# Performance work log

Hardware: AMD Instinct MI355X
Metric: run time of the kernel (lower is better)

Reference implementation:

```python
import jax, jax.numpy as jnp
import numpy as np

DIM = 1024
HEADS = 16
HEAD_DIM = DIM // HEADS
HIDDEN = 4 * DIM
SCALE = HEAD_DIM ** -0.5
EPS = 1e-5


def _layernorm(x, g, b):
    mu = jnp.mean(x, axis=-1, keepdims=True)
    var = jnp.mean(jnp.square(x - mu), axis=-1, keepdims=True)
    return (x - mu) * jax.lax.rsqrt(var + EPS) * g + b


def setup_inputs() -> dict:
    key = jax.random.key(0)
    ks = jax.random.split(key, 8)
    B, N, C = 4, 2048, DIM
    s = 0.02
    return {
        "x": jax.random.normal(ks[0], (B, N, C), dtype=jnp.float32),
        "ln1_g": jnp.ones((C,), jnp.float32),
        "ln1_b": jnp.zeros((C,), jnp.float32),
        "qkv_w": jax.random.normal(ks[1], (3 * C, C), jnp.float32) * s,
        "proj_w": jax.random.normal(ks[2], (C, C), jnp.float32) * s,
        "proj_b": jnp.zeros((C,), jnp.float32),
        "ln2_g": jnp.ones((C,), jnp.float32),
        "ln2_b": jnp.zeros((C,), jnp.float32),
        "fc1_w": jax.random.normal(ks[3], (HIDDEN, C), jnp.float32) * s,
        "fc1_b": jnp.zeros((HIDDEN,), jnp.float32),
        "fc2_w": jax.random.normal(ks[4], (C, HIDDEN), jnp.float32) * s,
        "fc2_b": jnp.zeros((C,), jnp.float32),
    }


def reference(x, ln1_g, ln1_b, qkv_w, proj_w, proj_b, ln2_g, ln2_b, fc1_w, fc1_b, fc2_w, fc2_b):
    B, N, C = x.shape
    # --- attention branch ---
    h = _layernorm(x, ln1_g, ln1_b)
    qkv = h @ qkv_w.T                                  # [B,N,3C]
    qkv = qkv.reshape(B, N, 3, HEADS, HEAD_DIM)
    q = qkv[:, :, 0].transpose(0, 2, 1, 3) * SCALE      # [B,H,N,D]
    k = qkv[:, :, 1].transpose(0, 2, 1, 3)
    v = qkv[:, :, 2].transpose(0, 2, 1, 3)
    attn = jax.nn.softmax(jnp.einsum('bhqd,bhkd->bhqk', q, k), axis=-1)
    o = jnp.einsum('bhqk,bhkd->bhqd', attn, v)          # [B,H,N,D]
    o = o.transpose(0, 2, 1, 3).reshape(B, N, C)
    x = x + (o @ proj_w.T + proj_b)
    # --- MLP branch ---
    h2 = _layernorm(x, ln2_g, ln2_b)
    h2 = jax.nn.gelu(h2 @ fc1_w.T + fc1_b, approximate=False)
    x = x + (h2 @ fc2_w.T + fc2_b)
    return x
```

## Files before the change

kernel.cpp:

```cpp
#include <hip/hip_runtime.h>
#include <math.h>

typedef __bf16 bf16;
typedef __attribute__((ext_vector_type(8))) __bf16 bf16x8;
typedef __attribute__((ext_vector_type(4))) __bf16 bf16x4;
typedef __attribute__((ext_vector_type(4))) float floatx4;

#define MFMA(a, b, c) __builtin_amdgcn_mfma_f32_16x16x32_bf16((a), (b), (c), 0, 0, 0)

__device__ __forceinline__ void async_load16(const bf16* g, bf16* l) {
    __builtin_amdgcn_global_load_lds((const __attribute__((address_space(1))) void*)(g),
                                     (__attribute__((address_space(3))) void*)(l), 16, 0, 0);
}

__global__ __launch_bounds__(256) void cast4_kernel(const float* __restrict__ a0,
                                                    const float* __restrict__ a1,
                                                    const float* __restrict__ a2,
                                                    const float* __restrict__ a3,
                                                    bf16* __restrict__ o0,
                                                    bf16* __restrict__ o1,
                                                    bf16* __restrict__ o2,
                                                    bf16* __restrict__ o3) {
    long i = (long)blockIdx.x * 256 + threadIdx.x;
    const float* in;
    bf16* out;
    long off;
    if (i < 393216) { in = a0; out = o0; off = i; }
    else if (i < 524288) { in = a1; out = o1; off = i - 393216; }
    else if (i < 1048576) { in = a2; out = o2; off = i - 524288; }
    else { in = a3; out = o3; off = i - 1048576; }
    const float4 a = ((const float4*)in)[2 * off];
    const float4 b = ((const float4*)in)[2 * off + 1];
    bf16x8 o;
    o[0] = (bf16)a.x; o[1] = (bf16)a.y; o[2] = (bf16)a.z; o[3] = (bf16)a.w;
    o[4] = (bf16)b.x; o[5] = (bf16)b.y; o[6] = (bf16)b.z; o[7] = (bf16)b.w;
    *(bf16x8*)(out + off * 8) = o;
}

__global__ __launch_bounds__(256) void ln_kernel(const float* __restrict__ x,
                                                 const float* __restrict__ g,
                                                 const float* __restrict__ b,
                                                 bf16* __restrict__ out) {
    const int row = blockIdx.x;
    const int tid = threadIdx.x;
    const float4 v = ((const float4*)(x + (long)row * 1024))[tid];
    float s  = v.x + v.y + v.z + v.w;
    float s2 = v.x * v.x + v.y * v.y + v.z * v.z + v.w * v.w;
#pragma unroll
    for (int off = 32; off > 0; off >>= 1) {
        s  += __shfl_xor(s, off, 64);
        s2 += __shfl_xor(s2, off, 64);
    }
    __shared__ float red[8];
    const int wave = tid >> 6, lane = tid & 63;
    if (lane == 0) { red[wave] = s; red[wave + 4] = s2; }
    __syncthreads();
    const float ts  = red[0] + red[1] + red[2] + red[3];
    const float ts2 = red[4] + red[5] + red[6] + red[7];
    const float mu   = ts * (1.0f / 1024.0f);
    const float rstd = rsqrtf(ts2 * (1.0f / 1024.0f) - mu * mu + 1e-5f);
    const float4 gg = ((const float4*)g)[tid];
    const float4 bb = ((const float4*)b)[tid];
    bf16x4 o;
    o[0] = (bf16)((v.x - mu) * rstd * gg.x + bb.x);
    o[1] = (bf16)((v.y - mu) * rstd * gg.y + bb.y);
    o[2] = (bf16)((v.z - mu) * rstd * gg.z + bb.z);
    o[3] = (bf16)((v.w - mu) * rstd * gg.w + bb.w);
    *(bf16x4*)(out + (long)row * 1024 + tid * 4) = o;
}

template <int EPI>
__global__ __launch_bounds__(256, 3)
void gemm_bt(const bf16* __restrict__ A, const bf16* __restrict__ B,
             const float* __restrict__ bias, const float* __restrict__ resid,
             void* __restrict__ Cout, bf16* __restrict__ vtout, int M, int N, int K) {
    __shared__ __align__(16) bf16 sA[128 * 64];
    __shared__ __align__(16) bf16 sB[128 * 64];
    const int tid  = threadIdx.x;
    const int lane = tid & 63;
    const int wave = tid >> 6;
    const int wm = (wave >> 1) << 6;
    const int wn = (wave & 1) << 6;
    const int c15 = lane & 15;
    const int kq  = lane >> 4;
    const int c7  = lane & 7;
    const long tileM = (long)blockIdx.y * 128;
    const long tileN = (long)blockIdx.x * 128;

    floatx4 acc[4][4] = {};

    const int srow = tid >> 3;
    const int scol = ((tid & 7) ^ (srow & 7)) * 8;
    const bf16* Abase = A + (tileM + srow) * (long)K + scol;
    const bf16* Bbase = B + (tileN + srow) * (long)K + scol;
    bf16* sAw = sA + tid * 8;
    bf16* sBw = sB + tid * 8;

    for (int k0 = 0; k0 < K; k0 += 64) {
        __syncthreads();
#pragma unroll
        for (int it = 0; it < 4; ++it) {
            async_load16(Abase + (long)it * 32 * K + k0, sAw + it * 2048);
            async_load16(Bbase + (long)it * 32 * K + k0, sBw + it * 2048);
        }
        __syncthreads();
#pragma unroll
        for (int kk = 0; kk < 2; ++kk) {
            bf16x8 a[4], b[4];
#pragma unroll
            for (int i = 0; i < 4; ++i) {
                const int ch = ((kk << 2) + kq) ^ c7;
                a[i] = *(const bf16x8*)(sA + (wm + i * 16 + c15) * 64 + ch * 8);
                b[i] = *(const bf16x8*)(sB + (wn + i * 16 + c15) * 64 + ch * 8);
            }
#pragma unroll
            for (int i = 0; i < 4; ++i)
#pragma unroll
                for (int j = 0; j < 4; ++j)
                    acc[i][j] = MFMA(a[i], b[j], acc[i][j]);
        }
    }

#pragma unroll
    for (int i = 0; i < 4; ++i)
#pragma unroll
        for (int j = 0; j < 4; ++j) {
            if (EPI == 3 && tileN >= 2048) {
                const long gnv  = tileN - 2048 + wn + j * 16 + c15;
                const long tokb = tileM + wm + i * 16 + kq * 4;
                const long row  = ((tokb >> 11) << 10) + gnv;
                bf16x4 ov;
#pragma unroll
                for (int r = 0; r < 4; ++r) ov[r] = (bf16)acc[i][j][r];
                *(bf16x4*)(vtout + row * 2048 + (tokb & 2047)) = ov;
            } else {
#pragma unroll
                for (int r = 0; r < 4; ++r) {
                    const long gm = tileM + wm + i * 16 + kq * 4 + r;
                    const long gn = tileN + wn + j * 16 + c15;
                    const float v = acc[i][j][r];
                    if (EPI == 0 || EPI == 3) {
                        ((bf16*)Cout)[gm * N + gn] = (bf16)v;
                    } else if (EPI == 1) {
                        ((float*)Cout)[gm * N + gn] = v + bias[gn] + resid[gm * N + gn];
                    } else {
                        const float t = v + bias[gn];
                        ((bf16*)Cout)[gm * N + gn] =
                            (bf16)(0.5f * t * (1.0f + erff(t * 0.70710678118654752f)));
                    }
                }
            }
        }
}

__global__ __launch_bounds__(256, 4)
void attn_kernel(const bf16* __restrict__ qkv, const bf16* __restrict__ vt,
                 bf16* __restrict__ o) {
    __shared__ __align__(16) bf16 sK[64 * 64];
    __shared__ __align__(16) bf16 sV[64 * 64];
    __shared__ __align__(16) bf16 sP[8][16 * 72];
    const int bh = blockIdx.x, b = bh >> 4, h = bh & 15;
    const int q0 = blockIdx.y * 128;
    const int tid = threadIdx.x, lane = tid & 63, wave = tid >> 6;
    const int c15 = lane & 15, kq = lane >> 4, c7 = lane & 7;

    bf16x8 qf[2][2];
#pragma unroll
    for (int t = 0; t < 2; ++t) {
        const bf16* qrow =
            qkv + ((long)(b * 2048 + q0 + wave * 32 + t * 16 + c15)) * 3072 + h * 64;
#pragma unroll
        for (int kk = 0; kk < 2; ++kk) {
            const bf16x8 raw = *(const bf16x8*)(qrow + kk * 32 + kq * 8);
            bf16x8 sc;
#pragma unroll
            for (int e = 0; e < 8; ++e) sc[e] = (bf16)((float)raw[e] * 0.18033688f);
            qf[t][kk] = sc;
        }
    }

    floatx4 oacc[2][4] = {};
    float l_s[2] = {0.f, 0.f};

    const bf16* kbase = qkv + ((long)b * 2048) * 3072 + 1024 + h * 64;
    const bf16* vbase = vt + (long)bh * 64 * 2048;

    const int srow = tid >> 3;
    const int scol = ((tid & 7) ^ (srow & 7)) * 8;
    bf16* sKw = sK + tid * 8;
    bf16* sVw = sV + tid * 8;
    bf16* sP0 = sP[wave * 2];
    bf16* sP1 = sP[wave * 2 + 1];

    for (int kv0 = 0; kv0 < 2048; kv0 += 64) {
        __syncthreads();
#pragma unroll
        for (int it = 0; it < 2; ++it) {
            async_load16(kbase + (long)(kv0 + it * 32 + srow) * 3072 + scol, sKw + it * 2048);
            async_load16(vbase + (long)(it * 32 + srow) * 2048 + kv0 + scol, sVw + it * 2048);
        }
        __syncthreads();

        floatx4 s0[4], s1[4];
#pragma unroll
        for (int j = 0; j < 4; ++j) {
            const bf16x8 k0 = *(const bf16x8*)(sK + (j * 16 + c15) * 64 + ((kq ^ c7) * 8));
            const bf16x8 k1 = *(const bf16x8*)(sK + (j * 16 + c15) * 64 + (((4 | kq) ^ c7) * 8));
            floatx4 a0 = {0.f, 0.f, 0.f, 0.f}, a1 = {0.f, 0.f, 0.f, 0.f};
            a0 = MFMA(k0, qf[0][0], a0);
            a0 = MFMA(k1, qf[0][1], a0);
            a1 = MFMA(k0, qf[1][0], a1);
            a1 = MFMA(k1, qf[1][1], a1);
            s0[j] = a0;
            s1[j] = a1;
        }

#pragma unroll
        for (int t = 0; t < 2; ++t) {
            floatx4* s = (t == 0) ? s0 : s1;
            bf16* sPt = (t == 0) ? sP0 : sP1;
            float rs = 0.f;
#pragma unroll
            for (int j = 0; j < 4; ++j) {
                const float p0 = __builtin_amdgcn_exp2f(s[j][0]);
                const float p1 = __builtin_amdgcn_exp2f(s[j][1]);
                const float p2 = __builtin_amdgcn_exp2f(s[j][2]);
                const float p3 = __builtin_amdgcn_exp2f(s[j][3]);
                rs += (p0 + p1) + (p2 + p3);
                bf16x4 pk;
                pk[0] = (bf16)p0; pk[1] = (bf16)p1; pk[2] = (bf16)p2; pk[3] = (bf16)p3;
                *(bf16x4*)(sPt + c15 * 72 + j * 16 + kq * 4) = pk;
            }
            l_s[t] += rs;
        }

        bf16x8 pf[2][2];
#pragma unroll
        for (int t = 0; t < 2; ++t) {
            bf16* sPt = (t == 0) ? sP0 : sP1;
            pf[t][0] = *(const bf16x8*)(sPt + c15 * 72 + kq * 8);
            pf[t][1] = *(const bf16x8*)(sPt + c15 * 72 + 32 + kq * 8);
        }
#pragma unroll
        for (int i = 0; i < 4; ++i) {
            const bf16x8 v0 = *(const bf16x8*)(sV + (i * 16 + c15) * 64 + ((kq ^ c7) * 8));
            const bf16x8 v1 = *(const bf16x8*)(sV + (i * 16 + c15) * 64 + (((4 | kq) ^ c7) * 8));
            oacc[0][i] = MFMA(v0, pf[0][0], oacc[0][i]);
            oacc[0][i] = MFMA(v1, pf[0][1], oacc[0][i]);
            oacc[1][i] = MFMA(v0, pf[1][0], oacc[1][i]);
            oacc[1][i] = MFMA(v1, pf[1][1], oacc[1][i]);
        }
    }

#pragma unroll
    for (int t = 0; t < 2; ++t) {
        float rs = l_s[t];
        rs += __shfl_xor(rs, 16, 64);
        rs += __shfl_xor(rs, 32, 64);
        const float linv = 1.0f / rs;
        const long tok = (long)(b * 2048 + q0 + wave * 32 + t * 16 + c15);
#pragma unroll
        for (int i = 0; i < 4; ++i) {
            bf16x4 ov;
#pragma unroll
            for (int r = 0; r < 4; ++r) ov[r] = (bf16)(oacc[t][i][r] * linv);
            *(bf16x4*)(o + tok * 1024 + h * 64 + i * 16 + kq * 4) = ov;
        }
    }
}

extern "C" void kernel_launch(void* const* d_in, const int* in_sizes, int n_in,
                              void* d_out, int out_size, void* d_ws, size_t ws_size,
                              hipStream_t stream) {
    const float* x      = (const float*)d_in[0];
    const float* ln1_g  = (const float*)d_in[1];
    const float* ln1_b  = (const float*)d_in[2];
    const float* qkv_w  = (const float*)d_in[3];
    const float* proj_w = (const float*)d_in[4];
    const float* proj_b = (const float*)d_in[5];
    const float* ln2_g  = (const float*)d_in[6];
    const float* ln2_b  = (const float*)d_in[7];
    const float* fc1_w  = (const float*)d_in[8];
    const float* fc1_b  = (const float*)d_in[9];
    const float* fc2_w  = (const float*)d_in[10];
    const float* fc2_b  = (const float*)d_in[11];
    float* out = (float*)d_out;

    char* ws = (char*)d_ws;
    bf16* actbuf = (bf16*)(ws);
    bf16* wqkv   = (bf16*)(ws + (16ull << 20));
    bf16* wproj  = (bf16*)(ws + (22ull << 20));
    bf16* wfc1   = (bf16*)(ws + (24ull << 20));
    bf16* wfc2   = (bf16*)(ws + (32ull << 20));
    bf16* qkvbuf = (bf16*)(ws + (40ull << 20));
    bf16* vtbuf  = (bf16*)(ws + (88ull << 20));
    bf16* gbuf   = (bf16*)(ws + (40ull << 20));

    const dim3 blk(256);

    cast4_kernel<<<6144, blk, 0, stream>>>(qkv_w, proj_w, fc1_w, fc2_w,
                                           wqkv, wproj, wfc1, wfc2);

    ln_kernel<<<8192, blk, 0, stream>>>(x, ln1_g, ln1_b, actbuf);

    gemm_bt<3><<<dim3(24, 64), blk, 0, stream>>>(actbuf, wqkv, nullptr, nullptr,
                                                 qkvbuf, vtbuf, 8192, 3072, 1024);
    attn_kernel<<<dim3(64, 16), blk, 0, stream>>>(qkvbuf, vtbuf, actbuf);

    gemm_bt<1><<<dim3(8, 64), blk, 0, stream>>>(actbuf, wproj, proj_b, x,
                                                d_out, nullptr, 8192, 1024, 1024);

    ln_kernel<<<8192, blk, 0, stream>>>(out, ln2_g, ln2_b, actbuf);

    gemm_bt<2><<<dim3(32, 64), blk, 0, stream>>>(actbuf, wfc1, fc1_b, nullptr,
                                                 gbuf, nullptr, 8192, 4096, 1024);
    gemm_bt<1><<<dim3(8, 64), blk, 0, stream>>>(gbuf, wfc2, fc2_b, out,
                                                d_out, nullptr, 8192, 1024, 4096);
}
```

Measured before the change: 496.6 us.

## Double-buffer attention K/V tiles and remap GEMM tiles across XCDs

The attention kernel now double-buffers its K and V shared-memory tiles. The async load for the next 64-key block is issued before computing on the current one, so global-to-LDS traffic can overlap with MFMA and softmax work. This doubles K/V LDS use, and the occupancy hint drops from 4 to 3 blocks per CU. The GEMM kernel also remaps its flat block index so that each XCD gets a contiguous range of N tiles, aiming for better L2 reuse of the B operand. The remap assumes the grid's x-dimension is a multiple of 8.

```diff
diff --git a/kernel.cpp b/kernel.cpp
--- a/kernel.cpp
+++ b/kernel.cpp
@@ -84,8 +84,15 @@
     const int c15 = lane & 15;
     const int kq  = lane >> 4;
     const int c7  = lane & 7;
-    const long tileM = (long)blockIdx.y * 128;
-    const long tileN = (long)blockIdx.x * 128;
+
+    const int flat  = blockIdx.y * gridDim.x + blockIdx.x;
+    const int xcd   = flat & 7;
+    const int local = flat >> 3;
+    const int ntX   = gridDim.x >> 3;
+    const int mtile = local / ntX;
+    const int ntile = xcd * ntX + (local - mtile * ntX);
+    const long tileM = (long)mtile * 128;
+    const long tileN = (long)ntile * 128;
 
     floatx4 acc[4][4] = {};
 
@@ -153,11 +160,11 @@
         }
 }
 
-__global__ __launch_bounds__(256, 4)
+__global__ __launch_bounds__(256, 3)
 void attn_kernel(const bf16* __restrict__ qkv, const bf16* __restrict__ vt,
                  bf16* __restrict__ o) {
-    __shared__ __align__(16) bf16 sK[64 * 64];
-    __shared__ __align__(16) bf16 sV[64 * 64];
+    __shared__ __align__(16) bf16 sK[2][64 * 64];
+    __shared__ __align__(16) bf16 sV[2][64 * 64];
     __shared__ __align__(16) bf16 sP[8][16 * 72];
     const int bh = blockIdx.x, b = bh >> 4, h = bh & 15;
     const int q0 = blockIdx.y * 128;
@@ -187,70 +194,85 @@
 
     const int srow = tid >> 3;
     const int scol = ((tid & 7) ^ (srow & 7)) * 8;
-    bf16* sKw = sK + tid * 8;
-    bf16* sVw = sV + tid * 8;
     bf16* sP0 = sP[wave * 2];
     bf16* sP1 = sP[wave * 2 + 1];
 
-    for (int kv0 = 0; kv0 < 2048; kv0 += 64) {
+#define ATTN_ISSUE(kv, buf)                                                              \
+    {                                                                                    \
+        bf16* sKw = sK[buf] + tid * 8;                                                   \
+        bf16* sVw = sV[buf] + tid * 8;                                                   \
+        _Pragma("unroll") for (int it = 0; it < 2; ++it) {                               \
+            async_load16(kbase + (long)((kv) + it * 32 + srow) * 3072 + scol,            \
+                         sKw + it * 2048);                                               \
+            async_load16(vbase + (long)(it * 32 + srow) * 2048 + (kv) + scol,            \
+                         sVw + it * 2048);                                               \
+        }                                                                                \
+    }
+
+#define ATTN_COMPUTE(buf)                                                                \
+    {                                                                                    \
+        const bf16* sKc = sK[buf];                                                       \
+        const bf16* sVc = sV[buf];                                                       \
+        floatx4 s0[4], s1[4];                                                            \
+        _Pragma("unroll") for (int j = 0; j < 4; ++j) {                                  \
+            const bf16x8 k0 =                                                            \
+                *(const bf16x8*)(sKc + (j * 16 + c15) * 64 + ((kq ^ c7) * 8));           \
+            const bf16x8 k1 =                                                            \
+                *(const bf16x8*)(sKc + (j * 16 + c15) * 64 + (((4 | kq) ^ c7) * 8));     \
+            floatx4 a0 = {0.f, 0.f, 0.f, 0.f}, a1 = {0.f, 0.f, 0.f, 0.f};                \
+            a0 = MFMA(k0, qf[0][0], a0);                                                 \
+            a0 = MFMA(k1, qf[0][1], a0);                                                 \
+            a1 = MFMA(k0, qf[1][0], a1);                                                 \
+            a1 = MFMA(k1, qf[1][1], a1);                                                 \
+            s0[j] = a0;                                                                  \
+            s1[j] = a1;                                                                  \
+        }                                                                                \
+        _Pragma("unroll") for (int t = 0; t < 2; ++t) {                                  \
+            floatx4* s = (t == 0) ? s0 : s1;                                             \
+            bf16* sPt = (t == 0) ? sP0 : sP1;                                            \
+            float rs = 0.f;                                                              \
+            _Pragma("unroll") for (int j = 0; j < 4; ++j) {                               \
+                const float p0 = __builtin_amdgcn_exp2f(s[j][0]);                        \
+                const float p1 = __builtin_amdgcn_exp2f(s[j][1]);                        \
+                const float p2 = __builtin_amdgcn_exp2f(s[j][2]);                        \
+                const float p3 = __builtin_amdgcn_exp2f(s[j][3]);                        \
+                rs += (p0 + p1) + (p2 + p3);                                             \
+                bf16x4 pk;                                                               \
+                pk[0] = (bf16)p0; pk[1] = (bf16)p1;                                      \
+                pk[2] = (bf16)p2; pk[3] = (bf16)p3;                                      \
+                *(bf16x4*)(sPt + c15 * 72 + j * 16 + kq * 4) = pk;                       \
+            }                                                                            \
+            l_s[t] += rs;                                                                \
+        }                                                                                \
+        bf16x8 pf[2][2];                                                                 \
+        _Pragma("unroll") for (int t = 0; t < 2; ++t) {                                  \
+            bf16* sPt = (t == 0) ? sP0 : sP1;                                            \
+            pf[t][0] = *(const bf16x8*)(sPt + c15 * 72 + kq * 8);                        \
+            pf[t][1] = *(const bf16x8*)(sPt + c15 * 72 + 32 + kq * 8);                   \
+        }                                                                                \
+        _Pragma("unroll") for (int i = 0; i < 4; ++i) {                                  \
+            const bf16x8 v0 =                                                            \
+                *(const bf16x8*)(sVc + (i * 16 + c15) * 64 + ((kq ^ c7) * 8));           \
+            const bf16x8 v1 =                                                            \
+                *(const bf16x8*)(sVc + (i * 16 + c15) * 64 + (((4 | kq) ^ c7) * 8));     \
+            oacc[0][i] = MFMA(v0, pf[0][0], oacc[0][i]);                                 \
+            oacc[0][i] = MFMA(v1, pf[0][1], oacc[0][i]);                                 \
+            oacc[1][i] = MFMA(v0, pf[1][0], oacc[1][i]);                                 \
+            oacc[1][i] = MFMA(v1, pf[1][1], oacc[1][i]);                                 \
+        }                                                                                \
+    }
+
+    ATTN_ISSUE(0, 0);
+    for (int kv0 = 0; kv0 < 2048; kv0 += 128) {
         __syncthreads();
-#pragma unroll
-        for (int it = 0; it < 2; ++it) {
-            async_load16(kbase + (long)(kv0 + it * 32 + srow) * 3072 + scol, sKw + it * 2048);
-            async_load16(vbase + (long)(it * 32 + srow) * 2048 + kv0 + scol, sVw + it * 2048);
-        }
+        if (kv0 + 64 < 2048) ATTN_ISSUE(kv0 + 64, 1);
+        ATTN_COMPUTE(0);
         __syncthreads();
-
-        floatx4 s0[4], s1[4];
-#pragma unroll
-        for (int j = 0; j < 4; ++j) {
-            const bf16x8 k0 = *(const bf16x8*)(sK + (j * 16 + c15) * 64 + ((kq ^ c7) * 8));
-            const bf16x8 k1 = *(const bf16x8*)(sK + (j * 16 + c15) * 64 + (((4 | kq) ^ c7) * 8));
-            floatx4 a0 = {0.f, 0.f, 0.f, 0.f}, a1 = {0.f, 0.f, 0.f, 0.f};
-            a0 = MFMA(k0, qf[0][0], a0);
-            a0 = MFMA(k1, qf[0][1], a0);
-            a1 = MFMA(k0, qf[1][0], a1);
-            a1 = MFMA(k1, qf[1][1], a1);
-            s0[j] = a0;
-            s1[j] = a1;
-        }
-
-#pragma unroll
-        for (int t = 0; t < 2; ++t) {
-            floatx4* s = (t == 0) ? s0 : s1;
-            bf16* sPt = (t == 0) ? sP0 : sP1;
-            float rs = 0.f;
-#pragma unroll
-            for (int j = 0; j < 4; ++j) {
-                const float p0 = __builtin_amdgcn_exp2f(s[j][0]);
-                const float p1 = __builtin_amdgcn_exp2f(s[j][1]);
-                const float p2 = __builtin_amdgcn_exp2f(s[j][2]);
-                const float p3 = __builtin_amdgcn_exp2f(s[j][3]);
-                rs += (p0 + p1) + (p2 + p3);
-                bf16x4 pk;
-                pk[0] = (bf16)p0; pk[1] = (bf16)p1; pk[2] = (bf16)p2; pk[3] = (bf16)p3;
-                *(bf16x4*)(sPt + c15 * 72 + j * 16 + kq * 4) = pk;
-            }
-            l_s[t] += rs;
-        }
-
-        bf16x8 pf[2][2];
-#pragma unroll
-        for (int t = 0; t < 2; ++t) {
-            bf16* sPt = (t == 0) ? sP0 : sP1;
-            pf[t][0] = *(const bf16x8*)(sPt + c15 * 72 + kq * 8);
-            pf[t][1] = *(const bf16x8*)(sPt + c15 * 72 + 32 + kq * 8);
-        }
-#pragma unroll
-        for (int i = 0; i < 4; ++i) {
-            const bf16x8 v0 = *(const bf16x8*)(sV + (i * 16 + c15) * 64 + ((kq ^ c7) * 8));
-            const bf16x8 v1 = *(const bf16x8*)(sV + (i * 16 + c15) * 64 + (((4 | kq) ^ c7) * 8));
-            oacc[0][i] = MFMA(v0, pf[0][0], oacc[0][i]);
-            oacc[0][i] = MFMA(v1, pf[0][1], oacc[0][i]);
-            oacc[1][i] = MFMA(v0, pf[1][0], oacc[1][i]);
-            oacc[1][i] = MFMA(v1, pf[1][1], oacc[1][i]);
-        }
-    }
+        if (kv0 + 128 < 2048) ATTN_ISSUE(kv0 + 128, 0);
+        ATTN_COMPUTE(1);
+    }
+#undef ATTN_ISSUE
+#undef ATTN_COMPUTE
 
 #pragma unroll
     for (int t = 0; t < 2; ++t) {
```

Measured after the change: 509.4 us. +2.6%, slower.
